# Performance work log

Hardware: AMD Instinct MI355X
Metric: run time of the kernel (lower is better)

The kernel has to match this reference:

```python
import jax, jax.numpy as jnp
import numpy as np

B, C, H, W = 8, 256, 64, 64
G = 32  # groups (channels % 32 == 0)
EPS = 1e-5


def setup_inputs() -> dict:
    key = jax.random.key(0)
    ks = jax.random.split(key, 6)
    x = jax.random.normal(ks[0], (B, C, H, W), dtype=jnp.float32)
    gamma = jnp.ones((C,), jnp.float32)
    beta = jnp.zeros((C,), jnp.float32)
    # xavier_normal for 1x1 convs: std = sqrt(2/(fan_in+fan_out))
    w_qkv = jax.random.normal(ks[1], (3 * C, C), dtype=jnp.float32) * np.sqrt(2.0 / (C + 3 * C))
    b_qkv = jnp.zeros((3 * C,), jnp.float32)
    w_proj = jax.random.normal(ks[2], (C, C), dtype=jnp.float32) * np.sqrt(2.0 / (C + C))
    b_proj = jnp.zeros((C,), jnp.float32)
    return {"x": x, "gamma": gamma, "beta": beta, "w_qkv": w_qkv,
            "b_qkv": b_qkv, "w_proj": w_proj, "b_proj": b_proj}


def reference(x, gamma, beta, w_qkv, b_qkv, w_proj, b_proj):
    b, c, hh, ww = x.shape
    n = hh * ww
    # GroupNorm over (C//G, H, W) per group
    xg = x.reshape(b, G, -1)
    mean = xg.mean(axis=-1, keepdims=True)
    var = xg.var(axis=-1, keepdims=True)
    h = ((xg - mean) / jnp.sqrt(var + EPS)).reshape(b, c, hh, ww)
    h = h * gamma[:, None, None] + beta[:, None, None]
    # 1x1 conv qkv projection as channel matmul
    qkv = jnp.einsum('bchw,oc->bohw', h, w_qkv) + b_qkv[:, None, None]
    q, k, v = jnp.split(qkv, 3, axis=1)  # each (B, C, H, W)
    q = q.reshape(b, c, n).transpose(0, 2, 1)  # (B, N, C)
    k = k.reshape(b, c, n)                     # (B, C, N)
    v = v.reshape(b, c, n).transpose(0, 2, 1)  # (B, N, C)
    attn = jax.nn.softmax(jnp.einsum('bnc,bcm->bnm', q, k) / jnp.sqrt(jnp.float32(c)), axis=-1)
    out = jnp.einsum('bnm,bmc->bnc', attn, v)  # (B, N, C)
    out = out.transpose(0, 2, 1).reshape(b, c, hh, ww)
    proj = jnp.einsum('bchw,oc->bohw', out, w_proj) + b_proj[:, None, None]
    return x + proj
```

## Files before the change

### kernel.cpp

```cpp
#include <hip/hip_runtime.h>
#include <stdint.h>

#define NB 8
#define NC 256
#define NHW 4096
#define NG 32
#define GELEMS (8*NHW)
#define EPS 1e-5f

typedef unsigned short u16;
typedef unsigned int u32;
typedef __attribute__((ext_vector_type(8))) short bf16x8;
typedef __attribute__((ext_vector_type(4))) float f32x4;
typedef __attribute__((ext_vector_type(16))) float f32x16;

__device__ __forceinline__ float bf2f(u16 u){ return __uint_as_float((u32)u << 16); }
__device__ __forceinline__ u16 f2bf(float f){
  u32 i = __float_as_uint(f);
  u32 r = i + 0x7fffu + ((i >> 16) & 1u);
  return (u16)(r >> 16);
}
__device__ __forceinline__ u32 pack2(float a, float b){
  return (u32)f2bf(a) | ((u32)f2bf(b) << 16);
}
__device__ __forceinline__ u32 cvtpk(float lo, float hi){
  u32 r;
  asm("v_cvt_pk_bf16_f32 %0, %1, %2" : "=v"(r) : "v"(lo), "v"(hi));
  return r;
}
__device__ __forceinline__ void plswap(u32 &a, u32 &b){
  asm volatile("v_permlane32_swap_b32 %0, %1" : "+v"(a), "+v"(b));
}

#define GLD16(g, l) __builtin_amdgcn_global_load_lds( \
    (const __attribute__((address_space(1))) u32*)(g), \
    (__attribute__((address_space(3))) u32*)(l), 16, 0, 0)

__global__ __launch_bounds__(256) void gn_stats_k(const float* __restrict__ x,
                                                  float* __restrict__ stats){
  int bg = blockIdx.x;
  const float* xp = x + (size_t)bg * GELEMS;
  float s = 0.f, s2 = 0.f;
  for (int i = threadIdx.x * 4; i < GELEMS; i += 256 * 4) {
    float4 v = *(const float4*)(xp + i);
    s  += v.x + v.y + v.z + v.w;
    s2 += v.x*v.x + v.y*v.y + v.z*v.z + v.w*v.w;
  }
  #pragma unroll
  for (int off = 32; off; off >>= 1) { s += __shfl_xor(s, off); s2 += __shfl_xor(s2, off); }
  __shared__ float rs[4], rs2[4];
  int w = threadIdx.x >> 6;
  if ((threadIdx.x & 63) == 0) { rs[w] = s; rs2[w] = s2; }
  __syncthreads();
  if (threadIdx.x == 0) {
    float ts = rs[0]+rs[1]+rs[2]+rs[3], t2 = rs2[0]+rs2[1]+rs2[2]+rs2[3];
    float mean = ts * (1.f/GELEMS);
    float var  = t2 * (1.f/GELEMS) - mean*mean;
    stats[2*bg]   = mean;
    stats[2*bg+1] = rsqrtf(var + EPS);
  }
}

__global__ __launch_bounds__(256) void gn_coef_k(const float* __restrict__ stats,
                                                 const float* __restrict__ gamma,
                                                 const float* __restrict__ beta,
                                                 float* __restrict__ coef){
  int i = blockIdx.x * 256 + threadIdx.x;
  if (i >= NB*NC) return;
  int b = i >> 8, c = i & 255;
  float mean = stats[2*(b*NG + (c>>3))];
  float rstd = stats[2*(b*NG + (c>>3)) + 1];
  float sc = gamma[c] * rstd;
  coef[2*i]   = sc;
  coef[2*i+1] = beta[c] - mean * sc;
}

__global__ __launch_bounds__(256) void cvtw_k(const float* __restrict__ w,
                                              u16* __restrict__ wbf){
  int i = blockIdx.x * 256 + threadIdx.x;
  wbf[i] = f2bf(w[i]);
}

__global__ __launch_bounds__(256) void cvtw2_k(const float* __restrict__ w,
                                               u16* __restrict__ wf){
  int i = blockIdx.x * 256 + threadIdx.x;
  int e = i & 7, chunk = i >> 3;
  int l = chunk & 63, ks = (chunk >> 6) & 15, ot = chunk >> 10;
  int c = ks*16 + (l>>5)*8 + e;
  int o = ot*32 + (l&31);
  wf[i] = f2bf(w[o*NC + c]);
}

__global__ __launch_bounds__(256, 2) void qkv_mfma_k(const float* __restrict__ x,
    const float* __restrict__ coef, const u16* __restrict__ wqbf,
    const float* __restrict__ b_qkv,
    u16* __restrict__ qT, u16* __restrict__ kF, u16* __restrict__ vF){
  __shared__ u16 Wbuf[2][4096];

  int bid = blockIdx.x;
  int wg = ((bid & 7) << 6) | (bid >> 3);
  int b  = wg >> 6;
  int n0 = (wg & 63) << 6;
  int w = threadIdx.x >> 6, lane = threadIdx.x & 63;
  int lo = lane & 15, g = lane >> 4;
  int n = n0 + w*16 + lo;

  int row1 = w*2 + (lane >> 5);
  int sxor = ((lane & 31) ^ (row1 & 7)) * 8;
  int src1 = row1 * 256 + sxor;
  int src2 = (row1 + 8) * 256 + sxor;

  auto STAGE = [&](int bufi, int ot) {
    const u16* src = wqbf + ot * 4096;
    GLD16(src + src1, &Wbuf[bufi][w * 512]);
    GLD16(src + src2, &Wbuf[bufi][2048 + w * 512]);
  };

  STAGE(0, 0);

  bf16x8 hf[8];
  {
    const float* xb = x + (size_t)b * NC * NHW + n;
    const float* cf = coef + b * 512;
    #pragma unroll
    for (int kc = 0; kc < 8; ++kc) {
      union { u32 u[4]; bf16x8 v; } hu;
      #pragma unroll
      for (int p = 0; p < 4; ++p) {
        int c = kc*32 + g*8 + p*2;
        float2 s0 = *(const float2*)(cf + 2*c);
        float2 s1 = *(const float2*)(cf + 2*c + 2);
        float f0 = xb[(size_t)c * NHW]     * s0.x + s0.y;
        float f1 = xb[(size_t)(c+1) * NHW] * s1.x + s1.y;
        hu.u[p] = pack2(f0, f1);
      }
      hf[kc] = hu.v;
    }
  }

  u16* qrow = qT + ((size_t)(b * NHW + n)) * NC;
  u16* kFb = kF + (size_t)b * NHW * NC;
  u16* vFb = vF + (size_t)b * NHW * NC;

  for (int ot = 0; ot < 48; ++ot) {
    __syncthreads();
    if (ot < 47) STAGE((ot + 1) & 1, ot + 1);
    const u16* Wl = Wbuf[ot & 1];
    int sw = lo & 7;
    f32x4 acc = (f32x4){0.f, 0.f, 0.f, 0.f};

    if (ot < 32) {
      #pragma unroll
      for (int kc = 0; kc < 8; ++kc) {
        bf16x8 wf = *(const bf16x8*)(Wl + lo*256 + ((kc*4 + g) ^ sw) * 8);
        acc = __builtin_amdgcn_mfma_f32_16x16x32_bf16(wf, hf[kc], acc, 0, 0, 0);
      }
      float4 bq = *(const float4*)(b_qkv + ot*16 + 4*g);
      float v0 = acc[0]+bq.x, v1 = acc[1]+bq.y, v2 = acc[2]+bq.z, v3 = acc[3]+bq.w;
      if (ot < 16) {
        v0 *= 0.0625f; v1 *= 0.0625f; v2 *= 0.0625f; v3 *= 0.0625f;
        uint2 st = { pack2(v0, v1), pack2(v2, v3) };
        *(uint2*)(qrow + ot*16 + 4*g) = st;
      } else {
        uint2 st = { pack2(v0, v1), pack2(v2, v3) };
        int cb = (ot-16)*16 + 4*g;
        int l = (n & 31) + 32*((cb >> 3) & 1);
        size_t addr = (((size_t)(n >> 5)*16 + (ot-16))*64 + l)*8 + (cb & 7);
        *(uint2*)(kFb + addr) = st;
      }
    } else {
      #pragma unroll
      for (int kc = 0; kc < 8; ++kc) {
        bf16x8 wf = *(const bf16x8*)(Wl + lo*256 + ((kc*4 + g) ^ sw) * 8);
        acc = __builtin_amdgcn_mfma_f32_16x16x32_bf16(hf[kc], wf, acc, 0, 0, 0);
      }
      int oc = (ot - 32) * 16 + lo;
      float bv = b_qkv[512 + oc];
      uint2 st = { pack2(acc[0]+bv, acc[1]+bv), pack2(acc[2]+bv, acc[3]+bv) };
      int m = n0 + w*16 + 4*g;
      int cv = ((oc >> 5) & 7) + 8*(w & 1);
      int l = (oc & 31) + 32*((w*2 + (g >> 1)) & 1);
      size_t addr = (((size_t)(m >> 5)*16 + cv)*64 + l)*8 + ((4*g) & 7);
      *(uint2*)(vFb + addr) = st;
    }
  }
}

__global__ __launch_bounds__(256) void qkv_scalar_k(const float* __restrict__ x,
                                             const float* __restrict__ coef,
                                             const float* __restrict__ w_qkv,
                                             const float* __restrict__ b_qkv,
                                             u16* __restrict__ qT, u16* __restrict__ kT,
                                             u16* __restrict__ vS){
  int idx0 = blockIdx.x;
  int idx = (idx0 >> 3) + (idx0 & 7) * 768;
  int og = idx % 48;
  int t  = idx / 48;
  int nc = t & 15;
  int b  = t >> 4;
  int n  = nc * 256 + threadIdx.x;
  const float* xb = x + (size_t)b * NC * NHW + n;
  const float* cf = coef + b * NC * 2;
  int ob = og * 16;
  float acc[16];
  #pragma unroll
  for (int j = 0; j < 16; ++j) acc[j] = b_qkv[ob + j];
  for (int c = 0; c < NC; ++c) {
    float h = xb[(size_t)c * NHW] * cf[2*c] + cf[2*c+1];
    const float* wr = w_qkv + (size_t)ob * NC + c;
    #pragma unroll
    for (int j = 0; j < 16; ++j) acc[j] += h * wr[(size_t)j * NC];
  }
  if (ob < 512) {
    float sc = (ob < 256) ? 0.0625f : 1.0f;
    union { u16 h[16]; uint4 q[2]; } u;
    #pragma unroll
    for (int j = 0; j < 16; ++j) u.h[j] = f2bf(acc[j] * sc);
    u16* p = (ob < 256) ? (qT + ((size_t)(b*NHW + n))*NC + ob)
                        : (kT + ((size_t)(b*NHW + n))*NC + (ob - 256));
    *(uint4*)p = u.q[0];
    *(uint4*)(p + 8) = u.q[1];
  } else {
    u16* p = vS + ((size_t)(b*NC) + (ob - 512)) * NHW + n;
    #pragma unroll
    for (int j = 0; j < 16; ++j) p[(size_t)j * NHW] = f2bf(acc[j]);
  }
}

__global__ __launch_bounds__(256, 2) void attn_split_k(
    const u16* __restrict__ qT, const u16* __restrict__ kF, const u16* __restrict__ vF,
    const u16* __restrict__ wprojF, float* __restrict__ Praw, float* __restrict__ lsum){
  __shared__ char smem[65536];

  int bid = blockIdx.x;
  int b = bid & 7;
  int u = bid >> 3;
  int rb = u >> 1, h2 = u & 1;
  int n0 = rb << 7;
  int w = threadIdx.x >> 6, lane = threadIdx.x & 63;
  int ln = lane & 31, hl = lane >> 5;

  const u16* qTb = qT + (size_t)b * NHW * NC;
  const u16* kFb = kF + (size_t)b * NHW * NC;
  const u16* vFb = vF + (size_t)b * NHW * NC;

  int nrow = n0 + w*32 + ln;
  bf16x8 qf[16];
  {
    const u16* qp = qTb + (size_t)nrow * NC + hl*8;
    #pragma unroll
    for (int kc = 0; kc < 16; ++kc) qf[kc] = *(const bf16x8*)(qp + kc*16);
  }

  auto STAGE = [&](int bi, int tile){
    const u16* kp = kFb + (size_t)tile * 8192;
    const u16* vp = vFb + (size_t)tile * 8192;
    char* kb = smem + bi*16384;
    char* vb = smem + 32768 + bi*16384;
    int off = threadIdx.x * 8;
    #pragma unroll
    for (int i = 0; i < 4; ++i) {
      GLD16(kp + off + i*2048, kb + threadIdx.x*16 + i*4096);
      GLD16(vp + off + i*2048, vb + threadIdx.x*16 + i*4096);
    }
  };

  f32x16 oacc[8];
  #pragma unroll
  for (int ct = 0; ct < 8; ++ct)
    oacc[ct] = (f32x16){0.f,0.f,0.f,0.f,0.f,0.f,0.f,0.f,0.f,0.f,0.f,0.f,0.f,0.f,0.f,0.f};
  float lrun = 0.f;

  STAGE(0, h2);
  __syncthreads();

  for (int it = 0; it < 64; ++it) {
    int cur = it & 1;
    if (it < 63) STAGE(cur ^ 1, 2*(it+1) + h2);
    const char* kb = smem + cur*16384;
    const char* vb = smem + 32768 + cur*16384;

    f32x16 st = (f32x16){0.f,0.f,0.f,0.f,0.f,0.f,0.f,0.f,0.f,0.f,0.f,0.f,0.f,0.f,0.f,0.f};
    #pragma unroll
    for (int kc = 0; kc < 16; ++kc) {
      bf16x8 kf = *(const bf16x8*)(kb + kc*1024 + lane*16);
      st = __builtin_amdgcn_mfma_f32_32x32x16_bf16(kf, qf[kc], st, 0, 0, 0);
    }

    float p[16];
    #pragma unroll
    for (int r = 0; r < 16; ++r) p[r] = __expf(st[r]);
    lrun += (((p[0]+p[1])+(p[2]+p[3])) + ((p[4]+p[5])+(p[6]+p[7])))
          + (((p[8]+p[9])+(p[10]+p[11])) + ((p[12]+p[13])+(p[14]+p[15])));

    u32 a0 = cvtpk(p[0],  p[1]),  a1 = cvtpk(p[2],  p[3]);
    u32 a2 = cvtpk(p[4],  p[5]),  a3 = cvtpk(p[6],  p[7]);
    u32 a4 = cvtpk(p[8],  p[9]),  a5 = cvtpk(p[10], p[11]);
    u32 a6 = cvtpk(p[12], p[13]), a7 = cvtpk(p[14], p[15]);
    plswap(a0, a2); plswap(a1, a3);
    plswap(a4, a6); plswap(a5, a7);
    union { u32 u[4]; bf16x8 v; } pa0, pa1;
    pa0.u[0]=a0; pa0.u[1]=a1; pa0.u[2]=a2; pa0.u[3]=a3;
    pa1.u[0]=a4; pa1.u[1]=a5; pa1.u[2]=a6; pa1.u[3]=a7;

    #pragma unroll
    for (int ks = 0; ks < 2; ++ks) {
      bf16x8 pa = ks ? pa1.v : pa0.v;
      #pragma unroll
      for (int ct = 0; ct < 8; ++ct) {
        bf16x8 vf = *(const bf16x8*)(vb + (ks*8 + ct)*1024 + lane*16);
        oacc[ct] = __builtin_amdgcn_mfma_f32_32x32x16_bf16(vf, pa, oacc[ct], 0, 0, 0);
      }
    }
    __syncthreads();
  }

  lrun += __shfl_xor(lrun, 32);
  if (lane < 32) lsum[((size_t)(h2*NB + b))*NHW + n0 + w*32 + lane] = lrun;

  u16* Ol = (u16*)(smem + w*16384);
  #pragma unroll
  for (int ct = 0; ct < 8; ++ct) {
    u32 c0 = cvtpk(oacc[ct][0],  oacc[ct][1]),  c1 = cvtpk(oacc[ct][2],  oacc[ct][3]);
    u32 c2 = cvtpk(oacc[ct][4],  oacc[ct][5]),  c3 = cvtpk(oacc[ct][6],  oacc[ct][7]);
    u32 c4 = cvtpk(oacc[ct][8],  oacc[ct][9]),  c5 = cvtpk(oacc[ct][10], oacc[ct][11]);
    u32 c6 = cvtpk(oacc[ct][12], oacc[ct][13]), c7 = cvtpk(oacc[ct][14], oacc[ct][15]);
    plswap(c0, c2); plswap(c1, c3);
    plswap(c4, c6); plswap(c5, c7);
    uint4 w0 = {c0, c1, c2, c3};
    uint4 w1 = {c4, c5, c6, c7};
    *(uint4*)(Ol + ln*256 + (((ct*4 + 0 + hl) ^ ln)) * 8) = w0;
    *(uint4*)(Ol + ln*256 + (((ct*4 + 2 + hl) ^ ln)) * 8) = w1;
  }

  f32x16 pacc[8];
  #pragma unroll
  for (int ot = 0; ot < 8; ++ot)
    pacc[ot] = (f32x16){0.f,0.f,0.f,0.f,0.f,0.f,0.f,0.f,0.f,0.f,0.f,0.f,0.f,0.f,0.f,0.f};
  #pragma unroll
  for (int ks = 0; ks < 16; ++ks) {
    bf16x8 af = *(const bf16x8*)(Ol + ln*256 + (((ks*2 + hl) ^ ln)) * 8);
    #pragma unroll
    for (int ot = 0; ot < 8; ++ot) {
      bf16x8 wf = *(const bf16x8*)(wprojF + ((size_t)(ot*16 + ks)*64 + lane) * 8);
      pacc[ot] = __builtin_amdgcn_mfma_f32_32x32x16_bf16(af, wf, pacc[ot], 0, 0, 0);
    }
  }
  float* Pr = Praw + ((size_t)(h2*NB + b)) * NHW * NC;
  #pragma unroll
  for (int ot = 0; ot < 8; ++ot) {
    int o = ot*32 + ln;
    #pragma unroll
    for (int r = 0; r < 16; ++r) {
      int n = n0 + w*32 + (r & 3) + 8*(r >> 2) + 4*hl;
      Pr[(size_t)n * NC + o] = pacc[ot][r];
    }
  }
}

__global__ __launch_bounds__(256) void s_k(const float* __restrict__ lsum,
                                           float* __restrict__ s){
  int i = blockIdx.x * 256 + threadIdx.x;
  s[i] = 1.f / (lsum[i] + lsum[(size_t)NB * NHW + i]);
}

__global__ __launch_bounds__(256) void combine_k(const float* __restrict__ x,
    const float* __restrict__ P0, const float* __restrict__ P1,
    const float* __restrict__ s, const float* __restrict__ b_proj,
    float* __restrict__ out){
  __shared__ float T[32 * 258];
  int bid = blockIdx.x;
  int b = bid & 7, nt = bid >> 3;
  int n0c = nt * 32;
  const float* p0 = P0 + ((size_t)b * NHW + n0c) * NC;
  const float* p1 = P1 + ((size_t)b * NHW + n0c) * NC;
  int t = threadIdx.x;
  int nl = t >> 3, fc0 = t & 7;
  #pragma unroll
  for (int j = 0; j < 8; ++j) {
    int fc = fc0 + 8*j;
    float4 a = *(const float4*)(p0 + nl*NC + fc*4);
    float4 c = *(const float4*)(p1 + nl*NC + fc*4);
    float* tp = T + nl*258 + fc*4;
    tp[0] = a.x + c.x; tp[1] = a.y + c.y; tp[2] = a.z + c.z; tp[3] = a.w + c.w;
  }
  int n = t & 31, og = t >> 5;
  float sv = s[b*NHW + n0c + n];
  __syncthreads();
  #pragma unroll 4
  for (int pass = 0; pass < 32; ++pass) {
    int o = pass*8 + og;
    size_t base = ((size_t)(b*NC + o))*NHW + n0c + n;
    out[base] = x[base] + b_proj[o] + sv * T[n*258 + o];
  }
}

__global__ __launch_bounds__(256, 2) void attn_fb_k(const float* __restrict__ x,
    const u16* __restrict__ qT, const u16* __restrict__ kT, const u16* __restrict__ vS,
    const float* __restrict__ w_proj, const float* __restrict__ b_proj,
    float* __restrict__ out){
  __shared__ char smem[73728];
  u16* Klds = (u16*)smem;
  u16* Vlds = (u16*)(smem + 32768);
  float* Olds = (float*)smem;

  int bid = blockIdx.x;
  int wg = ((bid & 7) << 6) | (bid >> 3);
  int b  = wg >> 6;
  int n0 = (wg & 63) << 6;
  int w = threadIdx.x >> 6, lane = threadIdx.x & 63;
  int lo = lane & 15, g = lane >> 4;
  int sw = lo & 7;

  const u16* qTb = qT + (size_t)b * NHW * NC;
  const u16* kTb = kT + (size_t)b * NHW * NC;
  const u16* vSb = vS + (size_t)b * NC * NHW;

  bf16x8 qf[8];
  {
    const u16* qp = qTb + (size_t)(n0 + w*16 + lo) * NC + g*8;
    #pragma unroll
    for (int kc = 0; kc < 8; ++kc) qf[kc] = *(const bf16x8*)(qp + kc*32);
  }

  int koff[8], voff[8];
  #pragma unroll
  for (int i = 0; i < 8; ++i) {
    int o = w*8192 + i*1024 + lane*16;
    int mr = o >> 9;
    int kch = ((o >> 4) & 31) ^ (mr & 7);
    koff[i] = mr*NC + kch*8;
    int cr = o >> 7;
    int vch = ((o >> 4) & 7) ^ (cr & 7);
    voff[i] = cr*NHW + vch*8;
  }

  f32x4 oacc[16];
  #pragma unroll
  for (int i = 0; i < 16; ++i) oacc[i] = (f32x4){0.f,0.f,0.f,0.f};
  float mrun = -1e30f, lrun = 0.f;

  char* Pw = smem + 65536 + w*2048;

  for (int m0 = 0; m0 < NHW; m0 += 64) {
    __syncthreads();
    const u16* kp = kTb + (size_t)m0 * NC;
    const u16* vp = vSb + m0;
    #pragma unroll
    for (int i = 0; i < 8; ++i) {
      GLD16(kp + koff[i], smem + w*8192 + i*1024);
      GLD16(vp + voff[i], smem + 32768 + w*8192 + i*1024);
    }
    __syncthreads();

    f32x4 st[4];
    #pragma unroll
    for (int mt = 0; mt < 4; ++mt) st[mt] = (f32x4){0.f,0.f,0.f,0.f};
    #pragma unroll
    for (int kc = 0; kc < 8; ++kc) {
      #pragma unroll
      for (int mt = 0; mt < 4; ++mt) {
        int ch = (kc*4 + g) ^ sw;
        bf16x8 kf = *(const bf16x8*)(Klds + (mt*16 + lo)*NC + ch*8);
        st[mt] = __builtin_amdgcn_mfma_f32_16x16x32_bf16(kf, qf[kc], st[mt], 0, 0, 0);
      }
    }

    float pmax = -1e30f;
    #pragma unroll
    for (int mt = 0; mt < 4; ++mt)
      #pragma unroll
      for (int r = 0; r < 4; ++r) pmax = fmaxf(pmax, st[mt][r]);
    pmax = fmaxf(pmax, __shfl_xor(pmax, 16));
    pmax = fmaxf(pmax, __shfl_xor(pmax, 32));

    if (!__all(pmax - mrun <= 8.f)) {
      float mnew = fmaxf(mrun, pmax);
      float corr = __expf(mrun - mnew);
      mrun = mnew;
      lrun *= corr;
      float c0 = __shfl(corr, 4*g+0), c1 = __shfl(corr, 4*g+1);
      float c2 = __shfl(corr, 4*g+2), c3 = __shfl(corr, 4*g+3);
      #pragma unroll
      for (int ct = 0; ct < 16; ++ct) {
        oacc[ct][0] *= c0; oacc[ct][1] *= c1; oacc[ct][2] *= c2; oacc[ct][3] *= c3;
      }
    }

    float psum = 0.f;
    #pragma unroll
    for (int mt = 0; mt < 4; ++mt) {
      float p0 = __expf(st[mt][0] - mrun);
      float p1 = __expf(st[mt][1] - mrun);
      float p2 = __expf(st[mt][2] - mrun);
      float p3 = __expf(st[mt][3] - mrun);
      psum += (p0 + p1) + (p2 + p3);
      uint2 pk = { pack2(p0, p1), pack2(p2, p3) };
      *(uint2*)(Pw + lo*128 + ((((2*mt + (g>>1)) ^ sw)) << 4) + ((g&1) << 3)) = pk;
    }
    psum += __shfl_xor(psum, 16);
    psum += __shfl_xor(psum, 32);
    lrun += psum;

    #pragma unroll
    for (int ks = 0; ks < 2; ++ks) {
      bf16x8 pa = *(const bf16x8*)(Pw + lo*128 + (((ks*4 + g) ^ sw) << 4));
      #pragma unroll
      for (int ct = 0; ct < 16; ++ct) {
        int ch = (ks*4 + g) ^ sw;
        bf16x8 vf = *(const bf16x8*)(Vlds + (ct*16 + lo)*64 + ch*8);
        oacc[ct] = __builtin_amdgcn_mfma_f32_16x16x32_bf16(pa, vf, oacc[ct], 0, 0, 0);
      }
    }
  }

  __syncthreads();
  float linv = 1.f / lrun;
  float l0 = __shfl(linv, 4*g+0), l1 = __shfl(linv, 4*g+1);
  float l2 = __shfl(linv, 4*g+2), l3 = __shfl(linv, 4*g+3);
  float* Ow = Olds + w*4096;
  #pragma unroll
  for (int ct = 0; ct < 16; ++ct) {
    int col = ct*16 + lo;
    Ow[(4*g+0)*256 + col] = oacc[ct][0] * l0;
    Ow[(4*g+1)*256 + col] = oacc[ct][1] * l1;
    Ow[(4*g+2)*256 + col] = oacc[ct][2] * l2;
    Ow[(4*g+3)*256 + col] = oacc[ct][3] * l3;
  }

  f32x4 pacc[16];
  #pragma unroll
  for (int i = 0; i < 16; ++i) pacc[i] = (f32x4){0.f,0.f,0.f,0.f};
  #pragma unroll
  for (int ks = 0; ks < 8; ++ks) {
    const float* ap = Ow + lo*256 + ks*32 + g*8;
    float4 a0 = *(const float4*)ap;
    float4 a1 = *(const float4*)(ap + 4);
    union { u16 h[8]; bf16x8 v; } au;
    au.h[0]=f2bf(a0.x); au.h[1]=f2bf(a0.y); au.h[2]=f2bf(a0.z); au.h[3]=f2bf(a0.w);
    au.h[4]=f2bf(a1.x); au.h[5]=f2bf(a1.y); au.h[6]=f2bf(a1.z); au.h[7]=f2bf(a1.w);
    bf16x8 af = au.v;
    #pragma unroll
    for (int ot = 0; ot < 16; ++ot) {
      const float* wp = w_proj + (size_t)(ot*16 + lo)*NC + ks*32 + g*8;
      float4 b0 = *(const float4*)wp;
      float4 b1 = *(const float4*)(wp + 4);
      union { u16 h[8]; bf16x8 v; } bu;
      bu.h[0]=f2bf(b0.x); bu.h[1]=f2bf(b0.y); bu.h[2]=f2bf(b0.z); bu.h[3]=f2bf(b0.w);
      bu.h[4]=f2bf(b1.x); bu.h[5]=f2bf(b1.y); bu.h[6]=f2bf(b1.z); bu.h[7]=f2bf(b1.w);
      pacc[ot] = __builtin_amdgcn_mfma_f32_16x16x32_bf16(af, bu.v, pacc[ot], 0, 0, 0);
    }
  }

  int nr = n0 + w*16 + 4*g;
  #pragma unroll
  for (int ot = 0; ot < 16; ++ot) {
    int o = ot*16 + lo;
    float bp = b_proj[o];
    size_t base = ((size_t)(b*NC + o)) * NHW + nr;
    float4 xr = *(const float4*)(x + base);
    float4 ov = { pacc[ot][0] + bp + xr.x, pacc[ot][1] + bp + xr.y,
                  pacc[ot][2] + bp + xr.z, pacc[ot][3] + bp + xr.w };
    *(float4*)(out + base) = ov;
  }
}

extern "C" void kernel_launch(void* const* d_in, const int* in_sizes, int n_in,
                              void* d_out, int out_size, void* d_ws, size_t ws_size,
                              hipStream_t stream) {
  const float* x      = (const float*)d_in[0];
  const float* gamma  = (const float*)d_in[1];
  const float* beta   = (const float*)d_in[2];
  const float* w_qkv  = (const float*)d_in[3];
  const float* b_qkv  = (const float*)d_in[4];
  const float* w_proj = (const float*)d_in[5];
  const float* b_proj = (const float*)d_in[6];
  float* out = (float*)d_out;

  char* p = (char*)d_ws;
  float* stats = (float*)p;
  float* coef  = stats + 2 * NB * NG;
  u16* qT = (u16*)(p + 18432);
  u16* kF = qT + (size_t)NB * NHW * NC;
  u16* vF = kF + (size_t)NB * NHW * NC;
  u16* wqbf = vF + (size_t)NB * NC * NHW;
  u16* wprojF = wqbf + 3 * NC * NC;
  size_t base_end = 18432 + (size_t)3 * NB * NHW * NC * 2
                  + (size_t)3 * NC * NC * 2 + (size_t)NC * NC * 2;
  float* Praw = (float*)(p + base_end);
  float* lsum = (float*)(p + base_end + (size_t)2*NB*NC*NHW*4);
  float* sbuf = lsum + (size_t)2*NB*NHW;
  size_t need_split = base_end + (size_t)2*NB*NC*NHW*4 + (size_t)3*NB*NHW*4;

  gn_stats_k<<<NB * NG, 256, 0, stream>>>(x, stats);
  gn_coef_k<<<(NB * NC + 255) / 256, 256, 0, stream>>>(stats, gamma, beta, coef);
  if (ws_size >= need_split) {
    cvtw2_k<<<NC * NC / 256, 256, 0, stream>>>(w_proj, wprojF);
    cvtw_k<<<3 * NC * NC / 256, 256, 0, stream>>>(w_qkv, wqbf);
    qkv_mfma_k<<<512, 256, 0, stream>>>(x, coef, wqbf, b_qkv, qT, kF, vF);
    attn_split_k<<<512, 256, 0, stream>>>(qT, kF, vF, wprojF, Praw, lsum);
    s_k<<<NB * NHW / 256, 256, 0, stream>>>(lsum, sbuf);
    combine_k<<<1024, 256, 0, stream>>>(x, Praw, Praw + (size_t)NB*NC*NHW,
                                        sbuf, b_proj, out);
  } else {
    qkv_scalar_k<<<NB * 16 * 48, 256, 0, stream>>>(x, coef, w_qkv, b_qkv, qT, kF, vF);
    attn_fb_k<<<512, 256, 0, stream>>>(x, qT, kF, vF, w_proj, b_proj, out);
  }
}
```

Before: 230.5 us.

## Process two 32-row query tiles per wave in split-K attention kernel

Each wave now handles 64 query rows (two 32-row tiles) instead of 32, so every K/V tile staged into shared memory feeds twice the MFMA work. The grid is halved to 256 blocks and launch bounds drop to one block per SM to make room for the doubled accumulators and Q fragments. This cuts K/V global and LDS traffic per query but raises register pressure and lowers occupancy, and 256 blocks may underfill the GPU's compute units.

After: 232.8 us. Within noise of the previous version (+1.0%).

```diff
diff --git a/kernel.cpp b/kernel.cpp
--- a/kernel.cpp
+++ b/kernel.cpp
@@ -227,7 +227,7 @@
   }
 }
 
-__global__ __launch_bounds__(256, 2) void attn_split_k(
+__global__ __launch_bounds__(256, 1) void attn_split_k(
     const u16* __restrict__ qT, const u16* __restrict__ kF, const u16* __restrict__ vF,
     const u16* __restrict__ wprojF, float* __restrict__ Praw, float* __restrict__ lsum){
   __shared__ char smem[65536];
@@ -236,7 +236,7 @@
   int b = bid & 7;
   int u = bid >> 3;
   int rb = u >> 1, h2 = u & 1;
-  int n0 = rb << 7;
+  int n0 = rb << 8;
   int w = threadIdx.x >> 6, lane = threadIdx.x & 63;
   int ln = lane & 31, hl = lane >> 5;
 
@@ -244,12 +244,12 @@
   const u16* kFb = kF + (size_t)b * NHW * NC;
   const u16* vFb = vF + (size_t)b * NHW * NC;
 
-  int nrow = n0 + w*32 + ln;
-  bf16x8 qf[16];
-  {
-    const u16* qp = qTb + (size_t)nrow * NC + hl*8;
-    #pragma unroll
-    for (int kc = 0; kc < 16; ++kc) qf[kc] = *(const bf16x8*)(qp + kc*16);
+  bf16x8 qf[2][16];
+  #pragma unroll
+  for (int nt = 0; nt < 2; ++nt) {
+    const u16* qp = qTb + (size_t)(n0 + w*64 + nt*32 + ln) * NC + hl*8;
+    #pragma unroll
+    for (int kc = 0; kc < 16; ++kc) qf[nt][kc] = *(const bf16x8*)(qp + kc*16);
   }
 
   auto STAGE = [&](int bi, int tile){
@@ -265,11 +265,13 @@
     }
   };
 
-  f32x16 oacc[8];
-  #pragma unroll
-  for (int ct = 0; ct < 8; ++ct)
-    oacc[ct] = (f32x16){0.f,0.f,0.f,0.f,0.f,0.f,0.f,0.f,0.f,0.f,0.f,0.f,0.f,0.f,0.f,0.f};
-  float lrun = 0.f;
+  f32x16 oacc[2][8];
+  #pragma unroll
+  for (int nt = 0; nt < 2; ++nt)
+    #pragma unroll
+    for (int ct = 0; ct < 8; ++ct)
+      oacc[nt][ct] = (f32x16){0.f,0.f,0.f,0.f,0.f,0.f,0.f,0.f,0.f,0.f,0.f,0.f,0.f,0.f,0.f,0.f};
+  float lrun0 = 0.f, lrun1 = 0.f;
 
   STAGE(0, h2);
   __syncthreads();
@@ -280,80 +282,110 @@
     const char* kb = smem + cur*16384;
     const char* vb = smem + 32768 + cur*16384;
 
-    f32x16 st = (f32x16){0.f,0.f,0.f,0.f,0.f,0.f,0.f,0.f,0.f,0.f,0.f,0.f,0.f,0.f,0.f,0.f};
+    f32x16 st0 = (f32x16){0.f,0.f,0.f,0.f,0.f,0.f,0.f,0.f,0.f,0.f,0.f,0.f,0.f,0.f,0.f,0.f};
+    f32x16 st1 = st0;
     #pragma unroll
     for (int kc = 0; kc < 16; ++kc) {
       bf16x8 kf = *(const bf16x8*)(kb + kc*1024 + lane*16);
-      st = __builtin_amdgcn_mfma_f32_32x32x16_bf16(kf, qf[kc], st, 0, 0, 0);
-    }
-
-    float p[16];
-    #pragma unroll
-    for (int r = 0; r < 16; ++r) p[r] = __expf(st[r]);
-    lrun += (((p[0]+p[1])+(p[2]+p[3])) + ((p[4]+p[5])+(p[6]+p[7])))
-          + (((p[8]+p[9])+(p[10]+p[11])) + ((p[12]+p[13])+(p[14]+p[15])));
-
-    u32 a0 = cvtpk(p[0],  p[1]),  a1 = cvtpk(p[2],  p[3]);
-    u32 a2 = cvtpk(p[4],  p[5]),  a3 = cvtpk(p[6],  p[7]);
-    u32 a4 = cvtpk(p[8],  p[9]),  a5 = cvtpk(p[10], p[11]);
-    u32 a6 = cvtpk(p[12], p[13]), a7 = cvtpk(p[14], p[15]);
-    plswap(a0, a2); plswap(a1, a3);
-    plswap(a4, a6); plswap(a5, a7);
-    union { u32 u[4]; bf16x8 v; } pa0, pa1;
-    pa0.u[0]=a0; pa0.u[1]=a1; pa0.u[2]=a2; pa0.u[3]=a3;
-    pa1.u[0]=a4; pa1.u[1]=a5; pa1.u[2]=a6; pa1.u[3]=a7;
+      st0 = __builtin_amdgcn_mfma_f32_32x32x16_bf16(kf, qf[0][kc], st0, 0, 0, 0);
+      st1 = __builtin_amdgcn_mfma_f32_32x32x16_bf16(kf, qf[1][kc], st1, 0, 0, 0);
+    }
+
+    bf16x8 paf[2][2];
+    {
+      float p[16];
+      #pragma unroll
+      for (int r = 0; r < 16; ++r) p[r] = __expf(st0[r]);
+      lrun0 += (((p[0]+p[1])+(p[2]+p[3])) + ((p[4]+p[5])+(p[6]+p[7])))
+             + (((p[8]+p[9])+(p[10]+p[11])) + ((p[12]+p[13])+(p[14]+p[15])));
+      u32 a0 = cvtpk(p[0],  p[1]),  a1 = cvtpk(p[2],  p[3]);
+      u32 a2 = cvtpk(p[4],  p[5]),  a3 = cvtpk(p[6],  p[7]);
+      u32 a4 = cvtpk(p[8],  p[9]),  a5 = cvtpk(p[10], p[11]);
+      u32 a6 = cvtpk(p[12], p[13]), a7 = cvtpk(p[14], p[15]);
+      plswap(a0, a2); plswap(a1, a3);
+      plswap(a4, a6); plswap(a5, a7);
+      union { u32 u[4]; bf16x8 v; } u0, u1;
+      u0.u[0]=a0; u0.u[1]=a1; u0.u[2]=a2; u0.u[3]=a3;
+      u1.u[0]=a4; u1.u[1]=a5; u1.u[2]=a6; u1.u[3]=a7;
+      paf[0][0] = u0.v; paf[0][1] = u1.v;
+    }
+    {
+      float p[16];
+      #pragma unroll
+      for (int r = 0; r < 16; ++r) p[r] = __expf(st1[r]);
+      lrun1 += (((p[0]+p[1])+(p[2]+p[3])) + ((p[4]+p[5])+(p[6]+p[7])))
+             + (((p[8]+p[9])+(p[10]+p[11])) + ((p[12]+p[13])+(p[14]+p[15])));
+      u32 a0 = cvtpk(p[0],  p[1]),  a1 = cvtpk(p[2],  p[3]);
+      u32 a2 = cvtpk(p[4],  p[5]),  a3 = cvtpk(p[6],  p[7]);
+      u32 a4 = cvtpk(p[8],  p[9]),  a5 = cvtpk(p[10], p[11]);
+      u32 a6 = cvtpk(p[12], p[13]), a7 = cvtpk(p[14], p[15]);
+      plswap(a0, a2); plswap(a1, a3);
+      plswap(a4, a6); plswap(a5, a7);
+      union { u32 u[4]; bf16x8 v; } u0, u1;
+      u0.u[0]=a0; u0.u[1]=a1; u0.u[2]=a2; u0.u[3]=a3;
+      u1.u[0]=a4; u1.u[1]=a5; u1.u[2]=a6; u1.u[3]=a7;
+      paf[1][0] = u0.v; paf[1][1] = u1.v;
+    }
 
     #pragma unroll
     for (int ks = 0; ks < 2; ++ks) {
-      bf16x8 pa = ks ? pa1.v : pa0.v;
       #pragma unroll
       for (int ct = 0; ct < 8; ++ct) {
         bf16x8 vf = *(const bf16x8*)(vb + (ks*8 + ct)*1024 + lane*16);
-        oacc[ct] = __builtin_amdgcn_mfma_f32_32x32x16_bf16(vf, pa, oacc[ct], 0, 0, 0);
+        oacc[0][ct] = __builtin_amdgcn_mfma_f32_32x32x16_bf16(vf, paf[0][ks], oacc[0][ct], 0, 0, 0);
+        oacc[1][ct] = __builtin_amdgcn_mfma_f32_32x32x16_bf16(vf, paf[1][ks], oacc[1][ct], 0, 0, 0);
       }
     }
     __syncthreads();
   }
 
-  lrun += __shfl_xor(lrun, 32);
-  if (lane < 32) lsum[((size_t)(h2*NB + b))*NHW + n0 + w*32 + lane] = lrun;
+  lrun0 += __shfl_xor(lrun0, 32);
+  lrun1 += __shfl_xor(lrun1, 32);
+  if (lane < 32) {
+    float* lp = lsum + ((size_t)(h2*NB + b))*NHW + n0 + w*64;
+    lp[lane] = lrun0;
+    lp[32 + lane] = lrun1;
+  }
 
   u16* Ol = (u16*)(smem + w*16384);
-  #pragma unroll
-  for (int ct = 0; ct < 8; ++ct) {
-    u32 c0 = cvtpk(oacc[ct][0],  oacc[ct][1]),  c1 = cvtpk(oacc[ct][2],  oacc[ct][3]);
-    u32 c2 = cvtpk(oacc[ct][4],  oacc[ct][5]),  c3 = cvtpk(oacc[ct][6],  oacc[ct][7]);
-    u32 c4 = cvtpk(oacc[ct][8],  oacc[ct][9]),  c5 = cvtpk(oacc[ct][10], oacc[ct][11]);
-    u32 c6 = cvtpk(oacc[ct][12], oacc[ct][13]), c7 = cvtpk(oacc[ct][14], oacc[ct][15]);
-    plswap(c0, c2); plswap(c1, c3);
-    plswap(c4, c6); plswap(c5, c7);
-    uint4 w0 = {c0, c1, c2, c3};
-    uint4 w1 = {c4, c5, c6, c7};
-    *(uint4*)(Ol + ln*256 + (((ct*4 + 0 + hl) ^ ln)) * 8) = w0;
-    *(uint4*)(Ol + ln*256 + (((ct*4 + 2 + hl) ^ ln)) * 8) = w1;
-  }
-
-  f32x16 pacc[8];
-  #pragma unroll
-  for (int ot = 0; ot < 8; ++ot)
-    pacc[ot] = (f32x16){0.f,0.f,0.f,0.f,0.f,0.f,0.f,0.f,0.f,0.f,0.f,0.f,0.f,0.f,0.f,0.f};
-  #pragma unroll
-  for (int ks = 0; ks < 16; ++ks) {
-    bf16x8 af = *(const bf16x8*)(Ol + ln*256 + (((ks*2 + hl) ^ ln)) * 8);
+  float* Pr = Praw + ((size_t)(h2*NB + b)) * NHW * NC;
+  #pragma unroll
+  for (int nt = 0; nt < 2; ++nt) {
+    #pragma unroll
+    for (int ct = 0; ct < 8; ++ct) {
+      u32 c0 = cvtpk(oacc[nt][ct][0],  oacc[nt][ct][1]),  c1 = cvtpk(oacc[nt][ct][2],  oacc[nt][ct][3]);
+      u32 c2 = cvtpk(oacc[nt][ct][4],  oacc[nt][ct][5]),  c3 = cvtpk(oacc[nt][ct][6],  oacc[nt][ct][7]);
+      u32 c4 = cvtpk(oacc[nt][ct][8],  oacc[nt][ct][9]),  c5 = cvtpk(oacc[nt][ct][10], oacc[nt][ct][11]);
+      u32 c6 = cvtpk(oacc[nt][ct][12], oacc[nt][ct][13]), c7 = cvtpk(oacc[nt][ct][14], oacc[nt][ct][15]);
+      plswap(c0, c2); plswap(c1, c3);
+      plswap(c4, c6); plswap(c5, c7);
+      uint4 w0 = {c0, c1, c2, c3};
+      uint4 w1 = {c4, c5, c6, c7};
+      *(uint4*)(Ol + ln*256 + (((ct*4 + 0 + hl) ^ ln)) * 8) = w0;
+      *(uint4*)(Ol + ln*256 + (((ct*4 + 2 + hl) ^ ln)) * 8) = w1;
+    }
+
+    f32x16 pacc[8];
+    #pragma unroll
+    for (int ot = 0; ot < 8; ++ot)
+      pacc[ot] = (f32x16){0.f,0.f,0.f,0.f,0.f,0.f,0.f,0.f,0.f,0.f,0.f,0.f,0.f,0.f,0.f,0.f};
+    #pragma unroll
+    for (int ks = 0; ks < 16; ++ks) {
+      bf16x8 af = *(const bf16x8*)(Ol + ln*256 + (((ks*2 + hl) ^ ln)) * 8);
+      #pragma unroll
+      for (int ot = 0; ot < 8; ++ot) {
+        bf16x8 wf = *(const bf16x8*)(wprojF + ((size_t)(ot*16 + ks)*64 + lane) * 8);
+        pacc[ot] = __builtin_amdgcn_mfma_f32_32x32x16_bf16(af, wf, pacc[ot], 0, 0, 0);
+      }
+    }
     #pragma unroll
     for (int ot = 0; ot < 8; ++ot) {
-      bf16x8 wf = *(const bf16x8*)(wprojF + ((size_t)(ot*16 + ks)*64 + lane) * 8);
-      pacc[ot] = __builtin_amdgcn_mfma_f32_32x32x16_bf16(af, wf, pacc[ot], 0, 0, 0);
-    }
-  }
-  float* Pr = Praw + ((size_t)(h2*NB + b)) * NHW * NC;
-  #pragma unroll
-  for (int ot = 0; ot < 8; ++ot) {
-    int o = ot*32 + ln;
-    #pragma unroll
-    for (int r = 0; r < 16; ++r) {
-      int n = n0 + w*32 + (r & 3) + 8*(r >> 2) + 4*hl;
-      Pr[(size_t)n * NC + o] = pacc[ot][r];
+      int o = ot*32 + ln;
+      #pragma unroll
+      for (int r = 0; r < 16; ++r) {
+        int n = n0 + w*64 + nt*32 + (r & 3) + 8*(r >> 2) + 4*hl;
+        Pr[(size_t)n * NC + o] = pacc[ot][r];
+      }
     }
   }
 }
@@ -598,7 +630,7 @@
     cvtw2_k<<<NC * NC / 256, 256, 0, stream>>>(w_proj, wprojF);
     cvtw_k<<<3 * NC * NC / 256, 256, 0, stream>>>(w_qkv, wqbf);
     qkv_mfma_k<<<512, 256, 0, stream>>>(x, coef, wqbf, b_qkv, qT, kF, vF);
-    attn_split_k<<<512, 256, 0, stream>>>(qT, kF, vF, wprojF, Praw, lsum);
+    attn_split_k<<<256, 256, 0, stream>>>(qT, kF, vF, wprojF, Praw, lsum);
     s_k<<<NB * NHW / 256, 256, 0, stream>>>(lsum, sbuf);
     combine_k<<<1024, 256, 0, stream>>>(x, Praw, Praw + (size_t)NB*NC*NHW,
                                         sbuf, b_proj, out);
```
